# Kernel tuning notes

Measured on AMD Instinct MI355X. Metric: run time of the kernel, lower is better.

The kernel has to match this reference:

```python
import jax, jax.numpy as jnp
import numpy as np

B, S, H, E, TOP_K = 4, 2048, 1024, 16, 4


def setup_inputs() -> dict:
    key = jax.random.key(0)
    ks = jax.random.split(key, 12)
    sc = 1.0 / np.sqrt(H)
    inp = {
        "x": jax.random.normal(ks[0], (B, S, H), dtype=jnp.float32),
        "image": jax.random.normal(ks[1], (B, S, H), dtype=jnp.float32),
        "text": jax.random.normal(ks[2], (B, S, H), dtype=jnp.float32),
        "audio": jax.random.normal(ks[3], (B, S, H), dtype=jnp.float32),
        # generalized router linear
        "Wg": jax.random.uniform(ks[4], (H, E), jnp.float32, -sc, sc),
        "bg": jax.random.uniform(ks[5], (E,), jnp.float32, -sc, sc),
        # per-modality router linears
        "Wi": jax.random.uniform(ks[6], (H, E), jnp.float32, -sc, sc),
        "bi": jax.random.uniform(ks[7], (E,), jnp.float32, -sc, sc),
        "Wt": jax.random.uniform(ks[8], (H, E), jnp.float32, -sc, sc),
        "bt": jax.random.uniform(ks[9], (E,), jnp.float32, -sc, sc),
        "Wa": jax.random.uniform(ks[10], (H, E), jnp.float32, -sc, sc),
        "ba": jax.random.uniform(ks[11], (E,), jnp.float32, -sc, sc),
    }
    return inp


def reference(x, image, text, audio, Wg, bg, Wi, bi, Wt, bt, Wa, ba):
    # combined_logits = generalized_router(x) + sum_m modality_router_m(modality_m)
    logits = (
        jnp.einsum("bsh,he->bse", x, Wg) + bg
        + jnp.einsum("bsh,he->bse", image, Wi) + bi
        + jnp.einsum("bsh,he->bse", text, Wt) + bt
        + jnp.einsum("bsh,he->bse", audio, Wa) + ba
    )  # [B,S,E]
    router_probs = jax.nn.softmax(logits, axis=-1)
    top_k_probs, top_k_indices = jax.lax.top_k(router_probs, TOP_K)
    top_k_probs = top_k_probs / jnp.sum(top_k_probs, axis=-1, keepdims=True)
    prob_per_expert = jnp.mean(router_probs, axis=(0, 1))  # [E]
    aux_loss = jnp.sum(prob_per_expert * jnp.log(prob_per_expert * E + 1e-9))
    return (top_k_indices, top_k_probs, aux_loss)
```

## Files before the change

kernel.cpp:

```cpp
#include <hip/hip_runtime.h>
#include <math.h>

constexpr int kTokens = 8192;
constexpr int kH      = 1024;
constexpr int kE      = 16;
constexpr int kTopK   = 4;
constexpr int kNC     = 16;

__global__ __launch_bounds__(256, 5)
void router_fmac(const float* __restrict__ x,   const float* __restrict__ img,
                 const float* __restrict__ txt, const float* __restrict__ aud,
                 const float* __restrict__ Wg,  const float* __restrict__ Wi,
                 const float* __restrict__ Wt,  const float* __restrict__ Wa,
                 float* __restrict__ partials)
{
    __shared__ float smem[5120];

    const int t  = threadIdx.x;
    const int w  = __builtin_amdgcn_readfirstlane(t >> 6);
    const int ln = t & 63;
    const int hs    = blockIdx.x & 15;
    const int tg    = blockIdx.x >> 4;
    const int tok0  = tg * 64;
    const int hbase = hs * 64;

    const float* Xs[4] = { x,  img, txt, aud };
    const float* Ws[4] = { Wg, Wi,  Wt,  Wa  };

    const int c2 = ln & 1;
    const int rA = ln >> 1;

    const size_t loff = (size_t)(tok0 + rA) * kH + hbase + w * 8 + c2 * 4;

    float* wb0 = smem + w * 512;
    float* wb1 = smem + 2048 + w * 512;

    float4 A0, A1, B0, B1, C0, C1;

#define ISSUE(Rx, Ry, p) { \
    const float* s_ = Xs[(p) >> 1] + loff + ((p) & 1) * 32; \
    Rx = *(const float4*)(s_); \
    Ry = *(const float4*)(s_ + (size_t)32 * kH); }

#define TWRITE(bufp, Rx, Ry) { \
    *(float4*)&(bufp)[rA * 8 + c2 * 4]        = Rx; \
    *(float4*)&(bufp)[(rA + 32) * 8 + c2 * 4] = Ry; }

#define FENCE() { asm volatile("s_waitcnt lgkmcnt(0)" ::: "memory"); \
                  __builtin_amdgcn_sched_barrier(0); }

    double dacc[kE];
#pragma unroll
    for (int e = 0; e < kE; ++e) dacc[e] = 0.0;
    float facc[kE];

#define RESET() { _Pragma("unroll") for (int e = 0; e < kE; ++e) facc[e] = 0.f; }
#define FOLD()  { _Pragma("unroll") for (int e = 0; e < kE; ++e) dacc[e] += (double)facc[e]; }

#define COMPUTE(bufp, p) { \
    const float* wbase = Ws[(p) >> 1] + (size_t)(hbase + ((p) & 1) * 32 + w * 8) * kE; \
    _Pragma("unroll") for (int k4 = 0; k4 < 2; ++k4) { \
        const float4 xv = *(const float4*)&(bufp)[ln * 8 + k4 * 4]; \
        _Pragma("unroll") for (int j = 0; j < 4; ++j) { \
            const float xh = (j == 0) ? xv.x : (j == 1) ? xv.y : (j == 2) ? xv.z : xv.w; \
            const float* wr = wbase + (k4 * 4 + j) * kE;    \
            const float4 w0 = *(const float4*)(wr + 0); \
            const float4 w1 = *(const float4*)(wr + 4); \
            const float4 w2 = *(const float4*)(wr + 8); \
            const float4 w3 = *(const float4*)(wr + 12); \
            facc[0]  += xh * w0.x;  facc[1]  += xh * w0.y; \
            facc[2]  += xh * w0.z;  facc[3]  += xh * w0.w; \
            facc[4]  += xh * w1.x;  facc[5]  += xh * w1.y; \
            facc[6]  += xh * w1.z;  facc[7]  += xh * w1.w; \
            facc[8]  += xh * w2.x;  facc[9]  += xh * w2.y; \
            facc[10] += xh * w2.z;  facc[11] += xh * w2.w; \
            facc[12] += xh * w3.x;  facc[13] += xh * w3.y; \
            facc[14] += xh * w3.z;  facc[15] += xh * w3.w; \
        } } }

    ISSUE(A0, A1, 0);  ISSUE(B0, B1, 1);  ISSUE(C0, C1, 2);
    TWRITE(wb0, A0, A1);
    FENCE();

    TWRITE(wb1, B0, B1);  ISSUE(A0, A1, 3);  RESET(); COMPUTE(wb0, 0);          FENCE();
    TWRITE(wb0, C0, C1);  ISSUE(B0, B1, 4);           COMPUTE(wb1, 1);  FOLD(); FENCE();
    TWRITE(wb1, A0, A1);  ISSUE(C0, C1, 5);  RESET(); COMPUTE(wb0, 2);          FENCE();
    TWRITE(wb0, B0, B1);  ISSUE(A0, A1, 6);           COMPUTE(wb1, 3);  FOLD(); FENCE();
    TWRITE(wb1, C0, C1);  ISSUE(B0, B1, 7);  RESET(); COMPUTE(wb0, 4);          FENCE();
    TWRITE(wb0, A0, A1);                              COMPUTE(wb1, 5);  FOLD(); FENCE();
    TWRITE(wb1, B0, B1);                     RESET(); COMPUTE(wb0, 6);          FENCE();
                                                      COMPUTE(wb1, 7);  FOLD();

#undef ISSUE
#undef TWRITE
#undef FENCE
#undef RESET
#undef FOLD
#undef COMPUTE

    __syncthreads();
#pragma unroll
    for (int q = 0; q < 4; ++q) {
        *(float4*)&smem[(w * 64 + ln) * 20 + q * 4] =
            make_float4((float)dacc[q * 4 + 0], (float)dacc[q * 4 + 1],
                        (float)dacc[q * 4 + 2], (float)dacc[q * 4 + 3]);
    }
    __syncthreads();
    {
        const int tok = t >> 2;
        const int eq  = t & 3;
        double s0 = 0.0, s1 = 0.0, s2 = 0.0, s3 = 0.0;
#pragma unroll
        for (int ww = 0; ww < 4; ++ww) {
            const float4 v = *(const float4*)&smem[(ww * 64 + tok) * 20 + eq * 4];
            s0 += (double)v.x;  s1 += (double)v.y;
            s2 += (double)v.z;  s3 += (double)v.w;
        }
        *(float4*)&partials[((size_t)(tok0 + tok) * kNC + hs) * kE + eq * 4] =
            make_float4((float)s0, (float)s1, (float)s2, (float)s3);
    }
}

__global__ __launch_bounds__(256)
void router_topk(const float* __restrict__ partials,
                 const float* __restrict__ bg, const float* __restrict__ bi,
                 const float* __restrict__ bt, const float* __restrict__ ba,
                 float* __restrict__ out, float* __restrict__ blocksum)
{
    __shared__ double lgs[32][2][kE + 2];
    __shared__ float  pr[32][kE + 1];

    const int t    = threadIdx.x;
    const int tq   = t >> 3;
    const int eq   = (t >> 1) & 3;
    const int hc   = t & 1;
    const int tok0 = blockIdx.x * 32;

    double a0 = 0.0, a1 = 0.0, a2 = 0.0, a3 = 0.0;
    if (hc == 0) {
        a0 = (double)bg[eq*4+0] + (double)bi[eq*4+0] + (double)bt[eq*4+0] + (double)ba[eq*4+0];
        a1 = (double)bg[eq*4+1] + (double)bi[eq*4+1] + (double)bt[eq*4+1] + (double)ba[eq*4+1];
        a2 = (double)bg[eq*4+2] + (double)bi[eq*4+2] + (double)bt[eq*4+2] + (double)ba[eq*4+2];
        a3 = (double)bg[eq*4+3] + (double)bi[eq*4+3] + (double)bt[eq*4+3] + (double)ba[eq*4+3];
    }

#pragma unroll
    for (int c8 = 0; c8 < 8; ++c8) {
        const int c = hc * 8 + c8;
        const float4 v = *(const float4*)(partials +
            ((size_t)(tok0 + tq) * kNC + c) * kE + eq * 4);
        a0 += (double)v.x;  a1 += (double)v.y;  a2 += (double)v.z;  a3 += (double)v.w;
    }
    lgs[tq][hc][eq*4+0] = a0;  lgs[tq][hc][eq*4+1] = a1;
    lgs[tq][hc][eq*4+2] = a2;  lgs[tq][hc][eq*4+3] = a3;
    __syncthreads();

    if (t < 32) {
        const int tok = tok0 + t;
        double lg[kE];
#pragma unroll
        for (int e = 0; e < kE; ++e) lg[e] = lgs[t][0][e] + lgs[t][1][e];

        double mx = lg[0];
#pragma unroll
        for (int e = 1; e < kE; ++e) mx = fmax(mx, lg[e]);

        float p[kE];
        float sum = 0.f;
#pragma unroll
        for (int e = 0; e < kE; ++e) {
            p[e] = expf((float)(lg[e] - mx));
            sum += p[e];
        }
        const float inv = 1.f / sum;
#pragma unroll
        for (int e = 0; e < kE; ++e) { p[e] *= inv; pr[t][e] = p[e]; }

        unsigned used = 0;
        float tp[kTopK];
        int   ti[kTopK];
        float s4 = 0.f;
#pragma unroll
        for (int k = 0; k < kTopK; ++k) {
            float best = -1.f;
            int   bidx = 0;
#pragma unroll
            for (int e = 0; e < kE; ++e) {
                if (!((used >> e) & 1u) && p[e] > best) { best = p[e]; bidx = e; }
            }
            used |= 1u << bidx;
            tp[k] = best;
            ti[k] = bidx;
            s4 += best;
        }
        const float rn = 1.f / s4;

        *(float4*)&out[(size_t)tok * kTopK] =
            make_float4((float)ti[0], (float)ti[1], (float)ti[2], (float)ti[3]);
        *(float4*)&out[(size_t)kTokens * kTopK + (size_t)tok * kTopK] =
            make_float4(tp[0] * rn, tp[1] * rn, tp[2] * rn, tp[3] * rn);
    }
    __syncthreads();

    if (t < kE) {
        float s = 0.f;
#pragma unroll
        for (int tk = 0; tk < 32; ++tk) s += pr[tk][t];
        blocksum[blockIdx.x * kE + t] = s;
    }
}

__global__ __launch_bounds__(256)
void router_aux(const float* __restrict__ blocksum, float* __restrict__ out)
{
    __shared__ double ps[16][kE];
    __shared__ double fin[kE];
    const int t = threadIdx.x;
    {
        const int e  = t & 15;
        const int bq = t >> 4;
        double s = 0.0;
#pragma unroll
        for (int k = 0; k < 16; ++k)
            s += (double)blocksum[(bq * 16 + k) * kE + e];
        ps[bq][e] = s;
    }
    __syncthreads();
    if (t < kE) {
        double s = 0.0;
#pragma unroll
        for (int q = 0; q < 16; ++q) s += ps[q][t];
        fin[t] = s / (double)kTokens;
    }
    __syncthreads();
    if (t == 0) {
        double aux = 0.0;
#pragma unroll
        for (int e = 0; e < kE; ++e) aux += fin[e] * log(fin[e] * (double)kE + 1e-9);
        out[(size_t)kTokens * kTopK * 2] = (float)aux;
    }
}

extern "C" void kernel_launch(void* const* d_in, const int* in_sizes, int n_in,
                              void* d_out, int out_size, void* d_ws, size_t ws_size,
                              hipStream_t stream)
{
    const float* x   = (const float*)d_in[0];
    const float* img = (const float*)d_in[1];
    const float* txt = (const float*)d_in[2];
    const float* aud = (const float*)d_in[3];
    const float* Wg  = (const float*)d_in[4];
    const float* bg  = (const float*)d_in[5];
    const float* Wi  = (const float*)d_in[6];
    const float* bi  = (const float*)d_in[7];
    const float* Wt  = (const float*)d_in[8];
    const float* bt  = (const float*)d_in[9];
    const float* Wa  = (const float*)d_in[10];
    const float* ba  = (const float*)d_in[11];

    float* out      = (float*)d_out;
    float* partials = (float*)d_ws;
    float* blocksum = (float*)((char*)d_ws + (size_t)kTokens * kNC * kE * 4);

    router_fmac<<<2048, 256, 0, stream>>>(x, img, txt, aud, Wg, Wi, Wt, Wa, partials);
    router_topk<<<256, 256, 0, stream>>>(partials, bg, bi, bt, ba, out, blocksum);
    router_aux<<<1, 256, 0, stream>>>(blocksum, out);
}
```

Measured before the change: 197.5 us.

## Stream activations directly into LDS via global_load_lds with swizzled 4-stage ring

```diff
diff --git a/kernel.cpp b/kernel.cpp
--- a/kernel.cpp
+++ b/kernel.cpp
@@ -6,6 +6,9 @@
 constexpr int kE      = 16;
 constexpr int kTopK   = 4;
 constexpr int kNC     = 16;
+
+typedef const float __attribute__((address_space(1))) ga_float;
+typedef float __attribute__((address_space(3))) lds_float;
 
 __global__ __launch_bounds__(256, 5)
 void router_fmac(const float* __restrict__ x,   const float* __restrict__ img,
@@ -14,7 +17,7 @@
                  const float* __restrict__ Wt,  const float* __restrict__ Wa,
                  float* __restrict__ partials)
 {
-    __shared__ float smem[5120];
+    __shared__ float smem[8192];
 
     const int t  = threadIdx.x;
     const int w  = __builtin_amdgcn_readfirstlane(t >> 6);
@@ -27,40 +30,37 @@
     const float* Xs[4] = { x,  img, txt, aud };
     const float* Ws[4] = { Wg, Wi,  Wt,  Wa  };
 
-    const int c2 = ln & 1;
-    const int rA = ln >> 1;
-
-    const size_t loff = (size_t)(tok0 + rA) * kH + hbase + w * 8 + c2 * 4;
-
-    float* wb0 = smem + w * 512;
-    float* wb1 = smem + 2048 + w * 512;
-
-    float4 A0, A1, B0, B1, C0, C1;
-
-#define ISSUE(Rx, Ry, p) { \
-    const float* s_ = Xs[(p) >> 1] + loff + ((p) & 1) * 32; \
-    Rx = *(const float4*)(s_); \
-    Ry = *(const float4*)(s_ + (size_t)32 * kH); }
-
-#define TWRITE(bufp, Rx, Ry) { \
-    *(float4*)&(bufp)[rA * 8 + c2 * 4]        = Rx; \
-    *(float4*)&(bufp)[(rA + 32) * 8 + c2 * 4] = Ry; }
-
-#define FENCE() { asm volatile("s_waitcnt lgkmcnt(0)" ::: "memory"); \
-                  __builtin_amdgcn_sched_barrier(0); }
+    const int drow = ln >> 3;
+    const int dcol = ((ln & 7) ^ drow) << 2;
+    const size_t soff0 = (size_t)(tok0 + w * 16 + drow)     * kH + hbase + dcol;
+    const size_t soff1 = (size_t)(tok0 + w * 16 + 8 + drow) * kH + hbase + dcol;
+
+#define ISSUE(p) { \
+    const float* xb_ = Xs[(p) >> 1] + ((p) & 1) * 32; \
+    float* d_ = smem + (((p) & 3) << 11) + (w << 9); \
+    __builtin_amdgcn_global_load_lds((ga_float*)(xb_ + soff0), \
+                                     (lds_float*)(d_),       16, 0, 0); \
+    __builtin_amdgcn_global_load_lds((ga_float*)(xb_ + soff1), \
+                                     (lds_float*)(d_ + 256), 16, 0, 0); }
+
+#define SYNCW(NSTR) { \
+    asm volatile("s_waitcnt vmcnt(" NSTR ")" ::: "memory"); \
+    __builtin_amdgcn_s_barrier(); \
+    asm volatile("" ::: "memory"); \
+    __builtin_amdgcn_sched_barrier(0); }
 
     double dacc[kE];
 #pragma unroll
     for (int e = 0; e < kE; ++e) dacc[e] = 0.0;
     float facc[kE];
 
-#define RESET() { _Pragma("unroll") for (int e = 0; e < kE; ++e) facc[e] = 0.f; }
-#define FOLD()  { _Pragma("unroll") for (int e = 0; e < kE; ++e) dacc[e] += (double)facc[e]; }
-
-#define COMPUTE(bufp, p) { \
+#define COMPUTE(p) { \
+    if (((p) & 1) == 0) { _Pragma("unroll") for (int e = 0; e < kE; ++e) facc[e] = 0.f; } \
+    const float* buf_  = smem + (((p) & 3) << 11) + ln * 32; \
     const float* wbase = Ws[(p) >> 1] + (size_t)(hbase + ((p) & 1) * 32 + w * 8) * kE; \
     _Pragma("unroll") for (int k4 = 0; k4 < 2; ++k4) { \
-        const float4 xv = *(const float4*)&(bufp)[ln * 8 + k4 * 4]; \
+        const int qs_ = ((w << 1) + k4) ^ (ln & 7); \
+        const float4 xv = *(const float4*)&buf_[qs_ << 2]; \
         _Pragma("unroll") for (int j = 0; j < 4; ++j) { \
             const float xh = (j == 0) ? xv.x : (j == 1) ? xv.y : (j == 2) ? xv.z : xv.w; \
             const float* wr = wbase + (k4 * 4 + j) * kE;    \
@@ -76,26 +76,22 @@
             facc[10] += xh * w2.z;  facc[11] += xh * w2.w; \
             facc[12] += xh * w3.x;  facc[13] += xh * w3.y; \
             facc[14] += xh * w3.z;  facc[15] += xh * w3.w; \
-        } } }
-
-    ISSUE(A0, A1, 0);  ISSUE(B0, B1, 1);  ISSUE(C0, C1, 2);
-    TWRITE(wb0, A0, A1);
-    FENCE();
-
-    TWRITE(wb1, B0, B1);  ISSUE(A0, A1, 3);  RESET(); COMPUTE(wb0, 0);          FENCE();
-    TWRITE(wb0, C0, C1);  ISSUE(B0, B1, 4);           COMPUTE(wb1, 1);  FOLD(); FENCE();
-    TWRITE(wb1, A0, A1);  ISSUE(C0, C1, 5);  RESET(); COMPUTE(wb0, 2);          FENCE();
-    TWRITE(wb0, B0, B1);  ISSUE(A0, A1, 6);           COMPUTE(wb1, 3);  FOLD(); FENCE();
-    TWRITE(wb1, C0, C1);  ISSUE(B0, B1, 7);  RESET(); COMPUTE(wb0, 4);          FENCE();
-    TWRITE(wb0, A0, A1);                              COMPUTE(wb1, 5);  FOLD(); FENCE();
-    TWRITE(wb1, B0, B1);                     RESET(); COMPUTE(wb0, 6);          FENCE();
-                                                      COMPUTE(wb1, 7);  FOLD();
+        } } \
+    if (((p) & 1) == 1) { _Pragma("unroll") for (int e = 0; e < kE; ++e) dacc[e] += (double)facc[e]; } }
+
+    ISSUE(0);  ISSUE(1);  ISSUE(2);
+    SYNCW("4");
+    ISSUE(3);  COMPUTE(0);  SYNCW("4");
+    ISSUE(4);  COMPUTE(1);  SYNCW("4");
+    ISSUE(5);  COMPUTE(2);  SYNCW("4");
+    ISSUE(6);  COMPUTE(3);  SYNCW("4");
+    ISSUE(7);  COMPUTE(4);  SYNCW("4");
+               COMPUTE(5);  SYNCW("2");
+               COMPUTE(6);  SYNCW("0");
+               COMPUTE(7);
 
 #undef ISSUE
-#undef TWRITE
-#undef FENCE
-#undef RESET
-#undef FOLD
+#undef SYNCW
 #undef COMPUTE
 
     __syncthreads();
```

Result: no change. 200.4 us (+1.5%).
